# Optimization experiments

Measured on AMD Instinct MI355X. Metric: run time of the kernel, lower is better.

## Reference

```python
import jax, jax.numpy as jnp
import numpy as np

N = 262144      # active input/output voxels
M = 131072      # neighbor pairs per kernel offset
K = 27          # kernel volume (3^3 hypercube)
C_IN = 32
C_OUT = 32


def setup_inputs() -> dict:
    key = jax.random.key(0)
    k1, k2, k3, k4, k5 = jax.random.split(key, 5)
    return {
        "input": jax.random.normal(k1, (N, C_IN), dtype=jnp.float32),
        "kernel": jax.random.normal(k2, (K, C_IN, C_OUT), dtype=jnp.float32) * 0.05,
        "bias": jax.random.normal(k3, (1, C_OUT), dtype=jnp.float32) * 0.05,
        "in_map": jax.random.randint(k4, (K, M), 0, N, dtype=jnp.int32),
        "out_map": jax.random.randint(k5, (K, M), 0, N, dtype=jnp.int32),
    }


def reference(input, kernel, bias, in_map, out_map):
    # Gather: [K, M, C_in] rows of input selected per kernel offset
    gathered = input[in_map]
    # Per-offset small GEMM: [K, M, C_in] x [K, C_in, C_out] -> [K, M, C_out]
    contrib = jnp.einsum('kmi,kio->kmo', gathered, kernel)
    # Scatter-add contributions into output rows
    out = jnp.zeros((N, C_OUT), dtype=input.dtype)
    out = out.at[out_map.reshape(-1)].add(contrib.reshape(-1, C_OUT))
    # Bias (has_bias=True)
    out = out + bias
    return out
```

## Files before the change

### kernel.cpp

```cpp
#include <hip/hip_runtime.h>


constexpr int N_VOX   = 262144;
constexpr int M_PAIRS = 131072;
constexpr int K_VOL   = 27;
constexpr int E_TOT   = K_VOL * M_PAIRS;
constexpr int NB      = 256;
constexpr int SCAP    = 640;
constexpr int SUBCAP  = 48;

typedef _Float16 h2  __attribute__((ext_vector_type(2)));
typedef _Float16 h4  __attribute__((ext_vector_type(4)));
typedef _Float16 h8  __attribute__((ext_vector_type(8)));
typedef float    f32x4 __attribute__((ext_vector_type(4)));

constexpr size_t WS_GCUR = 0;
constexpr size_t WS_WB   = 64 * 1024;
constexpr size_t WS_HIN  = (size_t)1 << 20;
constexpr size_t WS_SUB  = (size_t)18 << 20;

__device__ inline f32x4 mfma16x16x32(h8 a, h8 b, f32x4 c) {
    return __builtin_amdgcn_mfma_f32_16x16x32_f16(a, b, c, 0, 0, 0);
}
__device__ inline f32x4 mfma16x16x16(h4 a, h4 b, f32x4 c) {
    return __builtin_amdgcn_mfma_f32_16x16x16f16(a, b, c, 0, 0, 0);
}

__global__ __launch_bounds__(256) void convert_kernel(const float* __restrict__ in,
                                                      uint4* __restrict__ hin4) {
    if (blockIdx.x == 4096) {
        if (threadIdx.x < 4) hin4[(1u << 20) + threadIdx.x] = (uint4){0, 0, 0, 0};
        return;
    }
    const int idx = blockIdx.x * 256 + threadIdx.x;
    const float4* in4 = (const float4*)in;
    const float4 a = in4[2 * idx];
    const float4 b = in4[2 * idx + 1];
    h2 p0; p0[0] = (_Float16)a.x; p0[1] = (_Float16)a.y;
    h2 p1; p1[0] = (_Float16)a.z; p1[1] = (_Float16)a.w;
    h2 p2; p2[0] = (_Float16)b.x; p2[1] = (_Float16)b.y;
    h2 p3; p3[0] = (_Float16)b.z; p3[1] = (_Float16)b.w;
    uint4 v;
    v.x = __builtin_bit_cast(unsigned, p0);
    v.y = __builtin_bit_cast(unsigned, p1);
    v.z = __builtin_bit_cast(unsigned, p2);
    v.w = __builtin_bit_cast(unsigned, p3);
    hin4[idx] = v;
}

__global__ __launch_bounds__(256) void wprep_kernel(const float* __restrict__ kern,
                                                    unsigned short* __restrict__ wb) {
    const int idx = blockIdx.x * 256 + threadIdx.x;
    const int q  = idx & 7;
    const int l  = (idx >> 3) & 63;
    const int nt = (idx >> 9) & 1;
    const int k  = idx >> 10;
    const int kin = 8 * (l >> 4) + q;
    const int col = nt * 16 + (l & 15);
    const float w = kern[k * 1024 + kin * 32 + col];
    wb[idx] = __builtin_bit_cast(unsigned short, (_Float16)w);
}

__global__ __launch_bounds__(256) void bin_kernel(const int* __restrict__ in_map,
                                                  const int* __restrict__ out_map,
                                                  int* __restrict__ gcur,
                                                  int* __restrict__ subbuf) {
    __shared__ int lh[NB];
    const int t = threadIdx.x;
    lh[t] = 0;
    __syncthreads();

    const int k = (blockIdx.x * 4096) >> 17;
    int4 ivv[4], ovv[4];
    #pragma unroll
    for (int j = 0; j < 4; ++j) {
        const int i4 = blockIdx.x * 1024 + j * 256 + t;
        ivv[j] = ((const int4*)in_map)[i4];
        ovv[j] = ((const int4*)out_map)[i4];
    }
    #pragma unroll
    for (int j = 0; j < 4; ++j) {
        atomicAdd(&lh[ovv[j].x >> 10], 1);
        atomicAdd(&lh[ovv[j].y >> 10], 1);
        atomicAdd(&lh[ovv[j].z >> 10], 1);
        atomicAdd(&lh[ovv[j].w >> 10], 1);
    }
    __syncthreads();
    {
        const int c = lh[t];
        int base = 0;
        if (c > 0) base = atomicAdd(&gcur[t * K_VOL + k], c);
        __syncthreads();
        lh[t] = base;
    }
    __syncthreads();

    #pragma unroll
    for (int j = 0; j < 4; ++j) {
        int4 I = ivv[j], O = ovv[j];
        {
            const int b = O.x >> 10, p = (I.x << 10) | (O.x & 1023);
            const int pos = atomicAdd(&lh[b], 1);
            if (pos < SCAP) subbuf[(b * K_VOL + k) * SCAP + pos] = p;
        }
        {
            const int b = O.y >> 10, p = (I.y << 10) | (O.y & 1023);
            const int pos = atomicAdd(&lh[b], 1);
            if (pos < SCAP) subbuf[(b * K_VOL + k) * SCAP + pos] = p;
        }
        {
            const int b = O.z >> 10, p = (I.z << 10) | (O.z & 1023);
            const int pos = atomicAdd(&lh[b], 1);
            if (pos < SCAP) subbuf[(b * K_VOL + k) * SCAP + pos] = p;
        }
        {
            const int b = O.w >> 10, p = (I.w << 10) | (O.w & 1023);
            const int pos = atomicAdd(&lh[b], 1);
            if (pos < SCAP) subbuf[(b * K_VOL + k) * SCAP + pos] = p;
        }
    }
}

__global__ __launch_bounds__(256) void compute_kernel(
    const unsigned short* __restrict__ hin,
    const unsigned short* __restrict__ wb,
    const float* __restrict__ bias,
    const int*  __restrict__ gcur,
    const int*  __restrict__ subbuf,
    float* __restrict__ out)
{
    __shared__ int sub[4][SUBCAP];
    __shared__ int scnt[4];

    const int t      = threadIdx.x;
    const int l      = t & 63;
    const int w      = t >> 6;
    const int lane16 = l & 15;
    const int seg    = l >> 4;

    const int b = blockIdx.x >> 4;
    const int q = blockIdx.x & 15;

    const int SENT = N_VOX << 4;
    f32x4 acc0 = {0.f, 0.f, 0.f, 0.f};
    f32x4 acc1 = {0.f, 0.f, 0.f, 0.f};

    for (int k = 0; k < K_VOL; ++k) {
        if (t < 4) scnt[t] = 0;
        __syncthreads();

        const int nk = min(gcur[b * K_VOL + k], SCAP);
        const int* list = subbuf + (b * K_VOL + k) * SCAP;

        const uint4* wp = (const uint4*)wb + (k * 2) * 64 + l;
        const h8 B0 = __builtin_bit_cast(h8, wp[0]);
        const h8 B1 = __builtin_bit_cast(h8, wp[64]);

        for (int base = 0; base < nk; base += 256) {
            const int j = base + t;
            if (j < nk) {
                const int e   = list[j];
                const int o10 = e & 1023;
                const int g64 = o10 >> 4;
                if ((g64 >> 2) == q) {
                    const int wv  = g64 & 3;
                    const int pos = atomicAdd(&scnt[wv], 1);
                    if (pos < SUBCAP) sub[wv][pos] = ((e >> 10) << 4) | (o10 & 15);
                }
            }
        }
        __syncthreads();

        const int n = min(scnt[w], SUBCAP);
        for (int base = 0; base < n; base += 16) {
            const int slot = base + lane16;
            int es = (slot < n) ? sub[w][slot] : SENT;
            const uint4 a4 = *(const uint4*)(hin + (size_t)(es >> 4) * 32 + (seg << 3));
            const h8 A = __builtin_bit_cast(h8, a4);

            f32x4 ce0 = {0.f, 0.f, 0.f, 0.f};
            f32x4 ce1 = {0.f, 0.f, 0.f, 0.f};
            ce0 = mfma16x16x32(A, B0, ce0);
            ce1 = mfma16x16x32(A, B1, ce1);

            const int  pb = base + (seg << 2);
            const int4 e4 = *(const int4*)&sub[w][pb];
            h4 P;
            P[0] = (pb + 0 < n && (e4.x & 15) == lane16) ? (_Float16)1 : (_Float16)0;
            P[1] = (pb + 1 < n && (e4.y & 15) == lane16) ? (_Float16)1 : (_Float16)0;
            P[2] = (pb + 2 < n && (e4.z & 15) == lane16) ? (_Float16)1 : (_Float16)0;
            P[3] = (pb + 3 < n && (e4.w & 15) == lane16) ? (_Float16)1 : (_Float16)0;

            h4 b0, b1;
            b0[0] = (_Float16)ce0[0]; b0[1] = (_Float16)ce0[1];
            b0[2] = (_Float16)ce0[2]; b0[3] = (_Float16)ce0[3];
            b1[0] = (_Float16)ce1[0]; b1[1] = (_Float16)ce1[1];
            b1[2] = (_Float16)ce1[2]; b1[3] = (_Float16)ce1[3];

            acc0 = mfma16x16x16(P, b0, acc0);
            acc1 = mfma16x16x16(P, b1, acc1);
        }
        __syncthreads();
    }

    const int rowbase = blockIdx.x * 64 + w * 16 + seg * 4;
    const float bv0 = bias[lane16];
    const float bv1 = bias[16 + lane16];
    #pragma unroll
    for (int j = 0; j < 4; ++j) {
        out[(size_t)(rowbase + j) * 32 + lane16]      = acc0[j] + bv0;
        out[(size_t)(rowbase + j) * 32 + 16 + lane16] = acc1[j] + bv1;
    }
}

extern "C" void kernel_launch(void* const* d_in, const int* in_sizes, int n_in,
                              void* d_out, int out_size, void* d_ws, size_t ws_size,
                              hipStream_t stream) {
    const float* input   = (const float*)d_in[0];
    const float* kernel  = (const float*)d_in[1];
    const float* bias    = (const float*)d_in[2];
    const int*   in_map  = (const int*)d_in[3];
    const int*   out_map = (const int*)d_in[4];
    float* out = (float*)d_out;

    char* ws = (char*)d_ws;
    int* gcur            = (int*)(ws + WS_GCUR);
    unsigned short* wbuf = (unsigned short*)(ws + WS_WB);
    unsigned short* hin  = (unsigned short*)(ws + WS_HIN);
    int* subbuf          = (int*)(ws + WS_SUB);

    (void)hipMemsetAsync(gcur, 0, NB * K_VOL * sizeof(int), stream);
    convert_kernel<<<4097, 256, 0, stream>>>(input, (uint4*)hin);
    wprep_kernel  <<<108,  256, 0, stream>>>(kernel, wbuf);
    bin_kernel    <<<E_TOT / 4096, 256, 0, stream>>>(in_map, out_map, gcur, subbuf);
    compute_kernel<<<4096, 256, 0, stream>>>(hin, wbuf, bias, gcur, subbuf, out);
}
```

Baseline: 242.7 us.

## Process each output bin with one 1024-thread block instead of sixteen filtered blocks

The compute kernel now launches one 1024-thread block per 1024-voxel bin instead of 16 blocks of 256 threads. Each block reads the bin's pair list once per kernel offset and scatters entries into 64 per-window LDS sublists, and each wave handles four windows. This removes the 16x redundant reading and filtering of each list, and SUBCAP shrinks to 32. Gathers for out-of-range slots are now masked instead of reading a zeroed sentinel row, so the convert kernel no longer writes padding. In exchange the grid has far fewer blocks and fewer resident waves to hide gather latency, and a window holding more than 32 pairs for one offset would silently drop the extra pairs.

```diff
diff --git a/kernel.cpp b/kernel.cpp
--- a/kernel.cpp
+++ b/kernel.cpp
@@ -7,7 +7,7 @@
 constexpr int E_TOT   = K_VOL * M_PAIRS;
 constexpr int NB      = 256;
 constexpr int SCAP    = 640;
-constexpr int SUBCAP  = 48;
+constexpr int SUBCAP  = 32;
 
 typedef _Float16 h2  __attribute__((ext_vector_type(2)));
 typedef _Float16 h4  __attribute__((ext_vector_type(4)));
@@ -28,10 +28,6 @@
 
 __global__ __launch_bounds__(256) void convert_kernel(const float* __restrict__ in,
                                                       uint4* __restrict__ hin4) {
-    if (blockIdx.x == 4096) {
-        if (threadIdx.x < 4) hin4[(1u << 20) + threadIdx.x] = (uint4){0, 0, 0, 0};
-        return;
-    }
     const int idx = blockIdx.x * 256 + threadIdx.x;
     const float4* in4 = (const float4*)in;
     const float4 a = in4[2 * idx];
@@ -121,7 +117,7 @@
     }
 }
 
-__global__ __launch_bounds__(256) void compute_kernel(
+__global__ __launch_bounds__(1024) void compute_kernel(
     const unsigned short* __restrict__ hin,
     const unsigned short* __restrict__ wb,
     const float* __restrict__ bias,
@@ -129,24 +125,25 @@
     const int*  __restrict__ subbuf,
     float* __restrict__ out)
 {
-    __shared__ int sub[4][SUBCAP];
-    __shared__ int scnt[4];
+    __shared__ int sub[64][SUBCAP];
+    __shared__ int scnt[64];
 
     const int t      = threadIdx.x;
     const int l      = t & 63;
     const int w      = t >> 6;
     const int lane16 = l & 15;
     const int seg    = l >> 4;
-
-    const int b = blockIdx.x >> 4;
-    const int q = blockIdx.x & 15;
-
-    const int SENT = N_VOX << 4;
-    f32x4 acc0 = {0.f, 0.f, 0.f, 0.f};
-    f32x4 acc1 = {0.f, 0.f, 0.f, 0.f};
+    const int b      = blockIdx.x;
+
+    f32x4 acc0[4], acc1[4];
+    #pragma unroll
+    for (int s = 0; s < 4; ++s) {
+        acc0[s] = (f32x4){0.f, 0.f, 0.f, 0.f};
+        acc1[s] = (f32x4){0.f, 0.f, 0.f, 0.f};
+    }
 
     for (int k = 0; k < K_VOL; ++k) {
-        if (t < 4) scnt[t] = 0;
+        if (t < 64) scnt[t] = 0;
         __syncthreads();
 
         const int nk = min(gcur[b * K_VOL + k], SCAP);
@@ -156,60 +153,64 @@
         const h8 B0 = __builtin_bit_cast(h8, wp[0]);
         const h8 B1 = __builtin_bit_cast(h8, wp[64]);
 
-        for (int base = 0; base < nk; base += 256) {
-            const int j = base + t;
-            if (j < nk) {
-                const int e   = list[j];
-                const int o10 = e & 1023;
-                const int g64 = o10 >> 4;
-                if ((g64 >> 2) == q) {
-                    const int wv  = g64 & 3;
-                    const int pos = atomicAdd(&scnt[wv], 1);
-                    if (pos < SUBCAP) sub[wv][pos] = ((e >> 10) << 4) | (o10 & 15);
+        if (t < nk) {
+            const int e   = list[t];
+            const int o10 = e & 1023;
+            const int win = o10 >> 4;
+            const int pos = atomicAdd(&scnt[win], 1);
+            if (pos < SUBCAP) sub[win][pos] = ((e >> 10) << 4) | (o10 & 15);
+        }
+        __syncthreads();
+
+        #pragma unroll
+        for (int s = 0; s < 4; ++s) {
+            const int win = w * 4 + s;
+            const int n   = min(scnt[win], SUBCAP);
+            for (int base = 0; base < n; base += 16) {
+                const int slot = base + lane16;
+                h8 A = {};
+                if (slot < n) {
+                    const int es = sub[win][slot];
+                    const uint4 a4 = *(const uint4*)(hin + (size_t)(es >> 4) * 32 + (seg << 3));
+                    A = __builtin_bit_cast(h8, a4);
                 }
+
+                f32x4 ce0 = {0.f, 0.f, 0.f, 0.f};
+                f32x4 ce1 = {0.f, 0.f, 0.f, 0.f};
+                ce0 = mfma16x16x32(A, B0, ce0);
+                ce1 = mfma16x16x32(A, B1, ce1);
+
+                const int  pb = base + (seg << 2);
+                const int4 e4 = *(const int4*)&sub[win][pb & (SUBCAP - 4)];
+                h4 P;
+                P[0] = (pb + 0 < n && (e4.x & 15) == lane16) ? (_Float16)1 : (_Float16)0;
+                P[1] = (pb + 1 < n && (e4.y & 15) == lane16) ? (_Float16)1 : (_Float16)0;
+                P[2] = (pb + 2 < n && (e4.z & 15) == lane16) ? (_Float16)1 : (_Float16)0;
+                P[3] = (pb + 3 < n && (e4.w & 15) == lane16) ? (_Float16)1 : (_Float16)0;
+
+                h4 b0, b1;
+                b0[0] = (_Float16)ce0[0]; b0[1] = (_Float16)ce0[1];
+                b0[2] = (_Float16)ce0[2]; b0[3] = (_Float16)ce0[3];
+                b1[0] = (_Float16)ce1[0]; b1[1] = (_Float16)ce1[1];
+                b1[2] = (_Float16)ce1[2]; b1[3] = (_Float16)ce1[3];
+
+                acc0[s] = mfma16x16x16(P, b0, acc0[s]);
+                acc1[s] = mfma16x16x16(P, b1, acc1[s]);
             }
         }
         __syncthreads();
-
-        const int n = min(scnt[w], SUBCAP);
-        for (int base = 0; base < n; base += 16) {
-            const int slot = base + lane16;
-            int es = (slot < n) ? sub[w][slot] : SENT;
-            const uint4 a4 = *(const uint4*)(hin + (size_t)(es >> 4) * 32 + (seg << 3));
-            const h8 A = __builtin_bit_cast(h8, a4);
-
-            f32x4 ce0 = {0.f, 0.f, 0.f, 0.f};
-            f32x4 ce1 = {0.f, 0.f, 0.f, 0.f};
-            ce0 = mfma16x16x32(A, B0, ce0);
-            ce1 = mfma16x16x32(A, B1, ce1);
-
-            const int  pb = base + (seg << 2);
-            const int4 e4 = *(const int4*)&sub[w][pb];
-            h4 P;
-            P[0] = (pb + 0 < n && (e4.x & 15) == lane16) ? (_Float16)1 : (_Float16)0;
-            P[1] = (pb + 1 < n && (e4.y & 15) == lane16) ? (_Float16)1 : (_Float16)0;
-            P[2] = (pb + 2 < n && (e4.z & 15) == lane16) ? (_Float16)1 : (_Float16)0;
-            P[3] = (pb + 3 < n && (e4.w & 15) == lane16) ? (_Float16)1 : (_Float16)0;
-
-            h4 b0, b1;
-            b0[0] = (_Float16)ce0[0]; b0[1] = (_Float16)ce0[1];
-            b0[2] = (_Float16)ce0[2]; b0[3] = (_Float16)ce0[3];
-            b1[0] = (_Float16)ce1[0]; b1[1] = (_Float16)ce1[1];
-            b1[2] = (_Float16)ce1[2]; b1[3] = (_Float16)ce1[3];
-
-            acc0 = mfma16x16x16(P, b0, acc0);
-            acc1 = mfma16x16x16(P, b1, acc1);
-        }
-        __syncthreads();
-    }
-
-    const int rowbase = blockIdx.x * 64 + w * 16 + seg * 4;
+    }
+
     const float bv0 = bias[lane16];
     const float bv1 = bias[16 + lane16];
     #pragma unroll
-    for (int j = 0; j < 4; ++j) {
-        out[(size_t)(rowbase + j) * 32 + lane16]      = acc0[j] + bv0;
-        out[(size_t)(rowbase + j) * 32 + 16 + lane16] = acc1[j] + bv1;
+    for (int s = 0; s < 4; ++s) {
+        const int rowbase = b * 1024 + (w * 4 + s) * 16 + seg * 4;
+        #pragma unroll
+        for (int j = 0; j < 4; ++j) {
+            out[(size_t)(rowbase + j) * 32 + lane16]      = acc0[s][j] + bv0;
+            out[(size_t)(rowbase + j) * 32 + 16 + lane16] = acc1[s][j] + bv1;
+        }
     }
 }
 
@@ -230,8 +231,8 @@
     int* subbuf          = (int*)(ws + WS_SUB);
 
     (void)hipMemsetAsync(gcur, 0, NB * K_VOL * sizeof(int), stream);
-    convert_kernel<<<4097, 256, 0, stream>>>(input, (uint4*)hin);
+    convert_kernel<<<4096, 256, 0, stream>>>(input, (uint4*)hin);
     wprep_kernel  <<<108,  256, 0, stream>>>(kernel, wbuf);
     bin_kernel    <<<E_TOT / 4096, 256, 0, stream>>>(in_map, out_map, gcur, subbuf);
-    compute_kernel<<<4096, 256, 0, stream>>>(hin, wbuf, bias, gcur, subbuf, out);
-}
+    compute_kernel<<<NB, 1024, 0, stream>>>(hin, wbuf, bias, gcur, subbuf, out);
+}
```

New measurement: 231.4 us. -4.7%, faster.
